# Optimization experiments

Hardware: AMD Instinct MI355X
Metric: run time of the kernel (lower is better)

Reference implementation:

```python
import jax, jax.numpy as jnp
import numpy as np

D = 192
HEADS = 4
HD = D // HEADS
R = 3  # correlation radius actually used in forward_level
NDISP = (2 * R + 1) ** 2  # 49
T = 3  # frames -> 2 consecutive pairs
ITERS = 4


def layer_norm(x, w, b, eps=1e-5):
    m = jnp.mean(x, axis=-1, keepdims=True)
    v = jnp.var(x, axis=-1, keepdims=True)
    return (x - m) / jnp.sqrt(v + eps) * w + b


def mha(x, in_w, in_b, out_w, out_b):
    # torch nn.MultiheadAttention, batch_first, self-attention
    B, N, _ = x.shape
    qkv = x @ in_w.T + in_b
    q, k, v = jnp.split(qkv, 3, axis=-1)
    q = q.reshape(B, N, HEADS, HD).transpose(0, 2, 1, 3) * (1.0 / float(np.sqrt(HD)))
    k = k.reshape(B, N, HEADS, HD).transpose(0, 2, 1, 3)
    v = v.reshape(B, N, HEADS, HD).transpose(0, 2, 1, 3)
    att = jax.nn.softmax(jnp.einsum('bhqd,bhkd->bhqk', q, k), axis=-1)
    y = jnp.einsum('bhqk,bhkd->bhqd', att, v).transpose(0, 2, 1, 3).reshape(B, N, D)
    return y @ out_w.T + out_b


def tblock(x, p):
    ln1w, ln1b, inw, inb, ow, ob, ln2w, ln2b, w1, b1, w2, b2 = p
    x = x + mha(layer_norm(x, ln1w, ln1b), inw, inb, ow, ob)
    h = layer_norm(x, ln2w, ln2b)
    h = jax.nn.gelu(h @ w1.T + b1, approximate=False) @ w2.T + b2
    return x + h


def local_corr(f1, f2):
    C = f1.shape[1]
    scale = 1.0 / float(np.sqrt(C))
    outs = []
    for dy in range(-R, R + 1):
        for dx in range(-R, R + 1):
            f2s = jnp.roll(f2, (dy, dx), axis=(2, 3))
            outs.append(jnp.sum(f1 * f2s, axis=1) * scale)
    return jnp.stack(outs, axis=1)


def grid_sample_bilinear_border(img, grid):
    # img: B,C,H,W; grid: B,Ho,Wo,2 with (x,y) in [-1,1]; align_corners=True, border padding
    B, C, H, W = img.shape
    x = jnp.clip((grid[..., 0] + 1.0) * 0.5 * (W - 1), 0.0, W - 1)
    y = jnp.clip((grid[..., 1] + 1.0) * 0.5 * (H - 1), 0.0, H - 1)
    x0 = jnp.floor(x); y0 = jnp.floor(y)
    x1 = jnp.minimum(x0 + 1, W - 1); y1 = jnp.minimum(y0 + 1, H - 1)
    wx = (x - x0)[:, None]; wy = (y - y0)[:, None]
    imgf = img.reshape(B, C, H * W)
    Ho, Wo = x.shape[1], x.shape[2]
    def gather(yy, xx):
        idx = (yy * W + xx).astype(jnp.int32).reshape(B, 1, Ho * Wo)
        return jnp.take_along_axis(imgf, idx, axis=2).reshape(B, C, Ho, Wo)
    v00 = gather(y0, x0); v01 = gather(y0, x1)
    v10 = gather(y1, x0); v11 = gather(y1, x1)
    return v00 * (1 - wx) * (1 - wy) + v01 * wx * (1 - wy) + v10 * (1 - wx) * wy + v11 * wx * wy


def warp(img, flow):
    # flow in pixels, Bx2xHxW
    B, C, H, W = img.shape
    xs = jnp.linspace(-1.0, 1.0, W); ys = jnp.linspace(-1.0, 1.0, H)
    gx, gy = jnp.meshgrid(xs, ys)  # each (H, W), 'xy' indexing
    base = jnp.stack([gx, gy], axis=-1)[None]
    off = jnp.stack([flow[:, 0] * (2.0 / max(W - 1, 1)),
                     flow[:, 1] * (2.0 / max(H - 1, 1))], axis=-1)
    return grid_sample_bilinear_border(img, base + off)


def upsample2x_align(img):
    # F.interpolate(scale_factor=2, mode='bilinear', align_corners=True)
    B, C, H, W = img.shape
    Ho, Wo = 2 * H, 2 * W
    xs = jnp.linspace(-1.0, 1.0, Wo); ys = jnp.linspace(-1.0, 1.0, Ho)
    gx, gy = jnp.meshgrid(xs, ys)
    grid = jnp.broadcast_to(jnp.stack([gx, gy], axis=-1)[None], (B, Ho, Wo, 2))
    return grid_sample_bilinear_border(img, grid)


def conv2d(x, w, b):
    y = jax.lax.conv_general_dilated(x, w, (1, 1), ((1, 1), (1, 1)),
                                     dimension_numbers=('NCHW', 'OIHW', 'NCHW'))
    return y + b[None, :, None, None]


def _forward(feats_l1, feats_l2, feats_l3, tok_w, tok_b,
             lcm_ln1_w, lcm_ln1_b, lcm_in_w, lcm_in_b, lcm_out_w, lcm_out_b,
             lcm_ln2_w, lcm_ln2_b, lcm_mlp_w1, lcm_mlp_b1, lcm_mlp_w2, lcm_mlp_b2,
             gtr_ln1_w, gtr_ln1_b, gtr_in_w, gtr_in_b, gtr_out_w, gtr_out_b,
             gtr_ln2_w, gtr_ln2_b, gtr_mlp_w1, gtr_mlp_b1, gtr_mlp_w2, gtr_mlp_b2,
             head_w1, head_b1, head_w2, head_b2,
             ref1_w1, ref1_b1, ref1_w2, ref1_b2,
             ref0_w1, ref0_b1, ref0_w2, ref0_b2):
    feats = [[feats_l1[t] for t in range(T)],
             [feats_l2[t] for t in range(T)],
             [feats_l3[t] for t in range(T)]]
    # ---- CostTokenizer ----
    tokens = []
    for lvl in range(3):
        toks = []
        for k in range(T - 1):
            corr = local_corr(feats[lvl][k], feats[lvl][k + 1])
            toks.append(jnp.einsum('bchw,dc->bdhw', corr, tok_w[lvl]) + tok_b[lvl][None, :, None, None])
        tokens.append(toks)
    lcm_p = [(lcm_ln1_w[i], lcm_ln1_b[i], lcm_in_w[i], lcm_in_b[i], lcm_out_w[i], lcm_out_b[i],
              lcm_ln2_w[i], lcm_ln2_b[i], lcm_mlp_w1[i], lcm_mlp_b1[i], lcm_mlp_w2[i], lcm_mlp_b2[i])
             for i in range(lcm_ln1_w.shape[0])]
    gtr_p = [(gtr_ln1_w[i], gtr_ln1_b[i], gtr_in_w[i], gtr_in_b[i], gtr_out_w[i], gtr_out_b[i],
              gtr_ln2_w[i], gtr_ln2_b[i], gtr_mlp_w1[i], gtr_mlp_b1[i], gtr_mlp_w2[i], gtr_mlp_b2[i])
             for i in range(gtr_ln1_w.shape[0])]
    # ---- LatentCostMemory (EMA state; .detach() -> stop_gradient; state resets when N changes) ----
    state = None
    latent = []
    for toks in tokens:
        lvl_lat = []
        for tok in toks:
            B_, Dd, H, W = tok.shape
            x = tok.reshape(B_, Dd, H * W).transpose(0, 2, 1)  # b (h w) d
            for p in lcm_p:
                x = tblock(x, p)
            if state is None or state.shape[1] != x.shape[1]:
                state = jax.lax.stop_gradient(x)
            x = 0.8 * x + 0.2 * state
            state = jax.lax.stop_gradient(x)
            lvl_lat.append(x.transpose(0, 2, 1))  # b d n
        latent.append(lvl_lat)
    H8, W8 = feats[1][0].shape[-2:]
    coarse = []
    for lat in latent[1]:
        x = lat.transpose(0, 2, 1)
        for p in gtr_p:
            x = tblock(x, p)
        fv = jax.nn.gelu(x @ head_w1.T + head_b1, approximate=False) @ head_w2.T + head_b2
        coarse.append(fv.transpose(0, 2, 1).reshape(-1, 2, H8, W8))
    # ---- MSRecurrentDecoder ----
    outs = []
    for k, f8 in enumerate(coarse):
        cur = f8
        for _ in range(ITERS):
            w10 = warp(feats[1][k + 1], cur)
            x = jnp.concatenate([feats[1][k], cur, w10], axis=1)
            cur = cur + conv2d(jax.nn.gelu(conv2d(x, ref1_w1, ref1_b1), approximate=False), ref1_w2, ref1_b2)
        cur2 = upsample2x_align(cur)
        for _ in range(ITERS):
            w10 = warp(feats[0][k + 1], cur2)
            x = jnp.concatenate([feats[0][k], cur2, w10], axis=1)
            cur2 = cur2 + conv2d(jax.nn.gelu(conv2d(x, ref0_w1, ref0_b1), approximate=False), ref0_w2, ref0_b2)
        outs.append(cur2)
    return jnp.stack(outs)  # [pairs, B, 2, H/4, W/4]


def setup_inputs():
    key = jax.random.key(0)
    ks = iter(jax.random.split(key, 64))
    def rn(shape, s=1.0):
        return jax.random.normal(next(ks), shape, dtype=jnp.float32) * s
    B = 1
    inp = {}
    inp['feats_l1'] = rn((T, B, 64, 64, 64))
    inp['feats_l2'] = rn((T, B, 128, 32, 32))
    inp['feats_l3'] = rn((T, B, 192, 16, 16))
    inp['tok_w'] = rn((3, D, NDISP), 0.02)
    inp['tok_b'] = rn((3, D), 0.02)
    for pre, n in (('lcm', 6), ('gtr', 2)):
        inp[pre + '_ln1_w'] = jnp.ones((n, D), jnp.float32)
        inp[pre + '_ln1_b'] = jnp.zeros((n, D), jnp.float32)
        inp[pre + '_in_w'] = rn((n, 3 * D, D), 0.02)
        inp[pre + '_in_b'] = rn((n, 3 * D), 0.02)
        inp[pre + '_out_w'] = rn((n, D, D), 0.02)
        inp[pre + '_out_b'] = rn((n, D), 0.02)
        inp[pre + '_ln2_w'] = jnp.ones((n, D), jnp.float32)
        inp[pre + '_ln2_b'] = jnp.zeros((n, D), jnp.float32)
        inp[pre + '_mlp_w1'] = rn((n, 4 * D, D), 0.02)
        inp[pre + '_mlp_b1'] = rn((n, 4 * D), 0.02)
        inp[pre + '_mlp_w2'] = rn((n, D, 4 * D), 0.02)
        inp[pre + '_mlp_b2'] = rn((n, D), 0.02)
    inp['head_w1'] = rn((D, D), 0.02); inp['head_b1'] = rn((D,), 0.02)
    inp['head_w2'] = rn((2, D), 0.02); inp['head_b2'] = rn((2,), 0.02)
    inp['ref1_w1'] = rn((128, 258, 3, 3), 0.02); inp['ref1_b1'] = rn((128,), 0.02)
    inp['ref1_w2'] = rn((2, 128, 3, 3), 0.02); inp['ref1_b2'] = rn((2,), 0.02)
    inp['ref0_w1'] = rn((64, 130, 3, 3), 0.02); inp['ref0_b1'] = rn((64,), 0.02)
    inp['ref0_w2'] = rn((2, 64, 3, 3), 0.02); inp['ref0_b2'] = rn((2,), 0.02)
    return inp


def reference(feats_l1, feats_l2, feats_l3, tok_w, tok_b,
              lcm_ln1_w, lcm_ln1_b, lcm_in_w, lcm_in_b, lcm_out_w, lcm_out_b,
              lcm_ln2_w, lcm_ln2_b, lcm_mlp_w1, lcm_mlp_b1, lcm_mlp_w2, lcm_mlp_b2,
              gtr_ln1_w, gtr_ln1_b, gtr_in_w, gtr_in_b, gtr_out_w, gtr_out_b,
              gtr_ln2_w, gtr_ln2_b, gtr_mlp_w1, gtr_mlp_b1, gtr_mlp_w2, gtr_mlp_b2,
              head_w1, head_b1, head_w2, head_b2,
              ref1_w1, ref1_b1, ref1_w2, ref1_b2,
              ref0_w1, ref0_b1, ref0_w2, ref0_b2):
    return _forward(feats_l1, feats_l2, feats_l3, tok_w, tok_b,
                    lcm_ln1_w, lcm_ln1_b, lcm_in_w, lcm_in_b, lcm_out_w, lcm_out_b,
                    lcm_ln2_w, lcm_ln2_b, lcm_mlp_w1, lcm_mlp_b1, lcm_mlp_w2, lcm_mlp_b2,
                    gtr_ln1_w, gtr_ln1_b, gtr_in_w, gtr_in_b, gtr_out_w, gtr_out_b,
                    gtr_ln2_w, gtr_ln2_b, gtr_mlp_w1, gtr_mlp_b1, gtr_mlp_w2, gtr_mlp_b2,
                    head_w1, head_b1, head_w2, head_b2,
                    ref1_w1, ref1_b1, ref1_w2, ref1_b2,
                    ref0_w1, ref0_b1, ref0_w2, ref0_b2)
```

## Files before the change

kernel.cpp:

```cpp
#include <hip/hip_runtime.h>
#include <hip/hip_bf16.h>

typedef __hip_bfloat16 bf16;
typedef short bf16x8 __attribute__((ext_vector_type(8)));
typedef float f32x4 __attribute__((ext_vector_type(4)));

#define DEV __device__ __forceinline__

DEV float bf2f(bf16 v) { return __bfloat162float(v); }
DEV bf16 f2bf(float v) { return __float2bfloat16(v); }
DEV unsigned short bfr(float f) {
  bf16 h = __float2bfloat16(f);
  return *reinterpret_cast<unsigned short*>(&h);
}
DEV float shf(unsigned short u) {
  unsigned int x = ((unsigned int)u) << 16;
  return *reinterpret_cast<float*>(&x);
}
DEV float gelu_exact(float x) { return 0.5f * x * (1.0f + erff(x * 0.70710678118654752f)); }

DEV float ldw(const void* p, long i, int isb) {
  return isb ? __bfloat162float(((const bf16*)p)[i]) : ((const float*)p)[i];
}

__global__ void k_detect(const unsigned short* __restrict__ u, int* __restrict__ flag) {
  __shared__ int bad;
  if (threadIdx.x == 0) bad = 0;
  __syncthreads();
  for (int i = threadIdx.x; i < 8192; i += 256) {
    int expo = (u[i] >> 7) & 0xFF;
    if (expo >= 138) atomicOr(&bad, 1);
  }
  __syncthreads();
  if (threadIdx.x == 0) *flag = bad ? 0 : 1;
}
__global__ void k_setone(int* p) { *p = 1; }

__global__ void k_cvt(const void* __restrict__ s, float* __restrict__ d, int n,
                      const int* __restrict__ fl) {
  int isb = *fl;
  int i = blockIdx.x * blockDim.x + threadIdx.x;
  if (i < n) d[i] = ldw(s, i, isb);
}

__global__ void k_zerosh(unsigned short* __restrict__ p, int n8) {
  int i = blockIdx.x * blockDim.x + threadIdx.x;
  if (i < n8) { uint4 z = {0, 0, 0, 0}; *(uint4*)(p + (long)i * 8) = z; }
}

__global__ void k_padtokw(const void* __restrict__ tw, bf16* __restrict__ dst,
                          const int* __restrict__ fl) {
  int isb = *fl;
  int i = blockIdx.x * blockDim.x + threadIdx.x;
  if (i >= 12288) return;
  int n = i >> 6, k = i & 63;
  float v = (k < 49) ? ldw(tw, 9408 + (long)n * 49 + k, isb) : 0.0f;
  dst[i] = f2bf(v);
}

__global__ void k_packw(const void* __restrict__ src, bf16* __restrict__ dst,
                        int OC, int C, int ICT, int NP, int ICP, int n,
                        const int* __restrict__ fl) {
  int isb = *fl;
  int i = blockIdx.x * blockDim.x + threadIdx.x;
  if (i >= n) return;
  int s = i / (NP * ICP);
  int r = i - s * NP * ICP;
  int oc = r / ICP, icp = r - oc * ICP;
  float v = 0.0f;
  if (oc < OC) {
    int ic = -1;
    if (icp < C) ic = icp;
    else if (icp < 2 * C) ic = icp - C + C + 2;
    else if (icp < 2 * C + 2) ic = icp - 2 * C + C;
    if (ic >= 0 && ic < ICT) v = ldw(src, ((long)oc * ICT + ic) * 9 + s, isb);
  }
  dst[i] = f2bf(v);
}

__global__ void k_trans_feats(const void* __restrict__ in, bf16* __restrict__ Fp,
                              int F, int C, int HW, const int* __restrict__ fl) {
  int isb = *fl;
  int cpg = C >> 3;
  int n = F * HW * cpg;
  int i = blockIdx.x * blockDim.x + threadIdx.x;
  if (i >= n) return;
  int p = i % HW;
  int rem = i / HW;
  int c8 = rem % cpg;
  int f = rem / cpg;
  long base = (long)f * C * HW + (long)(c8 * 8) * HW + p;
  union { unsigned short u[8]; uint4 v; } pk;
#pragma unroll
  for (int j = 0; j < 8; ++j) pk.u[j] = bfr(ldw(in, base + (long)j * HW, isb));
  *(uint4*)((unsigned short*)Fp + ((long)f * HW + p) * C + c8 * 8) = pk.v;
}

__global__ void k_fill_feats(const bf16* __restrict__ Fp, bf16* __restrict__ Ap,
                             int C, int ICP, int H, int W) {
  int HW = H * W;
  int cpg = C >> 3;
  int n = 2 * HW * cpg;
  int i = blockIdx.x * blockDim.x + threadIdx.x;
  if (i >= n) return;
  int g = i % cpg;
  int rem = i / cpg;
  int p = rem % HW;
  int b = rem / HW;
  int h = p / W, w = p - h * W;
  const unsigned short* src = (const unsigned short*)Fp + ((long)b * HW + p) * C + g * 8;
  unsigned short* dst = (unsigned short*)Ap +
      ((long)b * (H + 2) * (W + 2) + (long)(h + 1) * (W + 2) + w + 1) * ICP + g * 8;
  *(uint4*)dst = *(const uint4*)src;
}

__global__ void k_warp_pack(const bf16* __restrict__ Fp, const float* __restrict__ flow,
                            bf16* __restrict__ Ap, int C, int ICP, int H, int W) {
  int HW = H * W;
  int cpg = C >> 3;
  int n = 2 * HW * cpg;
  int i = blockIdx.x * blockDim.x + threadIdx.x;
  if (i >= n) return;
  int g = i % cpg;
  int rem = i / cpg;
  int p = rem % HW;
  int b = rem / HW;
  int h = p / W, w = p - h * W;
  const float* fl = flow + (long)b * 2 * HW;
  float fx = fl[p], fy = fl[HW + p];
  unsigned short* drow = (unsigned short*)Ap +
      ((long)b * (H + 2) * (W + 2) + (long)(h + 1) * (W + 2) + w + 1) * ICP;
  if (g == 0) { drow[2 * C] = bfr(fx); drow[2 * C + 1] = bfr(fy); }
  float x = fminf(fmaxf((float)w + fx, 0.0f), (float)(W - 1));
  float y = fminf(fmaxf((float)h + fy, 0.0f), (float)(H - 1));
  int x0 = (int)floorf(x), y0 = (int)floorf(y);
  int x1 = min(x0 + 1, W - 1), y1 = min(y0 + 1, H - 1);
  float wx = x - (float)x0, wy = y - (float)y0;
  float w00 = (1 - wx) * (1 - wy), w01 = wx * (1 - wy);
  float w10 = (1 - wx) * wy, w11 = wx * wy;
  const unsigned short* f = (const unsigned short*)Fp + (long)(b + 1) * HW * C;
  int c = g * 8;
  union { unsigned short u[8]; uint4 v; } a = { .v = *(const uint4*)(f + (long)(y0 * W + x0) * C + c) };
  union { unsigned short u[8]; uint4 v; } bb = { .v = *(const uint4*)(f + (long)(y0 * W + x1) * C + c) };
  union { unsigned short u[8]; uint4 v; } cc = { .v = *(const uint4*)(f + (long)(y1 * W + x0) * C + c) };
  union { unsigned short u[8]; uint4 v; } dd = { .v = *(const uint4*)(f + (long)(y1 * W + x1) * C + c) };
  union { unsigned short u[8]; uint4 v; } o;
#pragma unroll
  for (int j = 0; j < 8; ++j) {
    float v = shf(a.u[j]) * w00 + shf(bb.u[j]) * w01 + shf(cc.u[j]) * w10 + shf(dd.u[j]) * w11;
    o.u[j] = bfr(v);
  }
  *(uint4*)(drow + C + c) = o.v;
}

template <int MW, int NT, int MODE>
__global__ __launch_bounds__(256) void k_conv_mfma(
    const bf16* __restrict__ Ap, int ICP, const bf16* __restrict__ Wp,
    const float* __restrict__ bias, const float* __restrict__ res,
    void* __restrict__ out, int NOUT, int H, int W, int lgW) {
  constexpr int NWN = 4 / MW;
  constexpr int BM = MW * 16;
  constexpr int BN = NWN * NT * 16;
  __shared__ unsigned short Asm[198][40];
  __shared__ unsigned short Wsm[9 * BN][40];
  int tid = threadIdx.x;
  int wv = tid >> 6, ln = tid & 63, quad = ln >> 4, l16 = ln & 15;
  int wm = wv % MW, wn = wv / MW;
  int n0 = blockIdx.x * BN;
  int m0 = blockIdx.y * BM;
  int b = blockIdx.z;
  int Wp2 = W + 2;
  int CW = (BM < W) ? BM : W;
  int lgCW = (CW == 64) ? 6 : 5;
  int RO = (BM > W) ? (BM >> lgW) : 1;
  int ACW = CW + 2;
  int AR = (RO + 2) * ACW;
  int py0 = m0 >> lgW;
  int px0 = m0 & (W - 1);
  const unsigned short* A = (const unsigned short*)Ap + (long)b * (H + 2) * Wp2 * ICP;
  int NPr = (MODE == 0) ? NOUT : 16;
  int nk = ICP >> 5;
  f32x4 acc[NT] = {};
  int mm_local = wm * 16 + l16;
  int plr = mm_local >> lgCW;
  int plc = mm_local & (CW - 1);
  for (int kc = 0; kc < nk; ++kc) {
    for (int i = tid; i < AR * 4; i += 256) {
      int r = i >> 2, c4 = i & 3;
      int sr = r / ACW, sc = r - sr * ACW;
      long g = ((long)(py0 + sr) * Wp2 + px0 + sc) * ICP + kc * 32 + c4 * 8;
      *(uint4*)&Asm[r][c4 * 8] = *(const uint4*)(A + g);
    }
    for (int i = tid; i < 9 * BN * 4; i += 256) {
      int r = i >> 2, c4 = i & 3;
      int s = r / BN, nl = r - s * BN;
      long g = ((long)s * NPr + n0 + nl) * ICP + kc * 32 + c4 * 8;
      *(uint4*)&Wsm[r][c4 * 8] = *(const uint4*)((const unsigned short*)Wp + g);
    }
    __syncthreads();
#pragma unroll
    for (int s = 0; s < 9; ++s) {
      int ky = s / 3, kx = s - ky * 3;
      bf16x8 af = *(const bf16x8*)&Asm[(plr + ky) * ACW + plc + kx][quad * 8];
#pragma unroll
      for (int nt = 0; nt < NT; ++nt) {
        bf16x8 wf = *(const bf16x8*)&Wsm[s * BN + (wn * NT + nt) * 16 + l16][quad * 8];
        acc[nt] = __builtin_amdgcn_mfma_f32_16x16x32_bf16(af, wf, acc[nt], 0, 0, 0);
      }
    }
    __syncthreads();
  }
  if (MODE == 0) {
#pragma unroll
    for (int nt = 0; nt < NT; ++nt) {
      int n = n0 + (wn * NT + nt) * 16 + l16;
      float bv = bias[n];
#pragma unroll
      for (int r = 0; r < 4; ++r) {
        int mmo = m0 + wm * 16 + quad * 4 + r;
        int py = mmo >> lgW, px = mmo & (W - 1);
        float v = gelu_exact(acc[nt][r] + bv);
        ((unsigned short*)out)[((long)b * (H + 2) * Wp2 + (long)(py + 1) * Wp2 + px + 1) * NOUT + n]
            = bfr(v);
      }
    }
  } else {
    int n = l16;
    if (wn == 0 && n < 2) {
      float bv = bias[n];
      int HW = H * W;
#pragma unroll
      for (int r = 0; r < 4; ++r) {
        int mmo = m0 + wm * 16 + quad * 4 + r;
        float v = acc[0][r] + bv + res[(long)b * 2 * HW + (long)n * HW + mmo];
        ((float*)out)[(long)b * 2 * HW + (long)n * HW + mmo] = v;
      }
    }
  }
}

__global__ void k_corr(const bf16* __restrict__ Fp2, bf16* __restrict__ corrT) {
  __shared__ unsigned short f1r[128];
  int p = blockIdx.x;
  int b = blockIdx.y;
  int t = threadIdx.x;
  const unsigned short* f1 = (const unsigned short*)Fp2 + ((long)b * 1024 + p) * 128;
  if (t < 16) *(uint4*)&f1r[t * 8] = *(const uint4*)(f1 + t * 8);
  __syncthreads();
  long rowo = ((long)b * 1024 + p) * 64;
  if (t < 49) {
    int dy = t / 7 - 3, dx = t % 7 - 3;
    int h = p >> 5, w = p & 31;
    int p2 = (((h - dy) & 31) << 5) | ((w - dx) & 31);
    const unsigned short* f2 = (const unsigned short*)Fp2 + ((long)(b + 1) * 1024 + p2) * 128;
    float s = 0.0f;
    for (int c = 0; c < 128; c += 8) {
      union { unsigned short u[8]; uint4 v; } av = { .v = *(const uint4*)&f1r[c] };
      union { unsigned short u[8]; uint4 v; } bv = { .v = *(const uint4*)(f2 + c) };
#pragma unroll
      for (int j = 0; j < 8; ++j) s += shf(av.u[j]) * shf(bv.u[j]);
    }
    corrT[rowo + t] = f2bf(s * 0.08838834764831845f);
  } else {
    corrT[rowo + t] = f2bf(0.0f);
  }
}

__global__ __launch_bounds__(256) void k_ln(const float* __restrict__ src, bf16* __restrict__ dst,
                     const void* __restrict__ w, long woff,
                     const void* __restrict__ b, long boff,
                     const int* __restrict__ fl) {
  int isb = *fl;
  int row = blockIdx.x * 4 + (threadIdx.x >> 6);
  int t = threadIdx.x & 63;
  const float* s = src + (long)row * 192;
  float e0 = s[t], e1 = s[t + 64], e2 = s[t + 128];
  float sum = e0 + e1 + e2;
  for (int o = 32; o; o >>= 1) sum += __shfl_xor(sum, o);
  float mean = sum * (1.0f / 192.0f);
  float d0 = e0 - mean, d1 = e1 - mean, d2 = e2 - mean;
  float vs = d0 * d0 + d1 * d1 + d2 * d2;
  for (int o = 32; o; o >>= 1) vs += __shfl_xor(vs, o);
  float rstd = rsqrtf(vs * (1.0f / 192.0f) + 1e-5f);
  bf16* o_ = dst + (long)row * 192;
  o_[t]       = f2bf(d0 * rstd * ldw(w, woff + t, isb)       + ldw(b, boff + t, isb));
  o_[t + 64]  = f2bf(d1 * rstd * ldw(w, woff + t + 64, isb)  + ldw(b, boff + t + 64, isb));
  o_[t + 128] = f2bf(d2 * rstd * ldw(w, woff + t + 128, isb) + ldw(b, boff + t + 128, isb));
}

template <int ACT, bool HASRES, int AMODE, int OUTBF, int VT>
__global__ __launch_bounds__(256) void k_gemm_mfma(
    const void* __restrict__ A, const void* __restrict__ W, long woff,
    const void* __restrict__ bias, long boff, const int* __restrict__ flb,
    const float* __restrict__ res, void* __restrict__ C,
    int M, int N, int K, const int* __restrict__ fl,
    const unsigned short* __restrict__ mop, const float* __restrict__ mml,
    bf16* __restrict__ vtout) {
  int isb = *fl;
  __shared__ unsigned short Asm[64][40];
  __shared__ unsigned short Wsm[64][40];
  int tid = threadIdx.x;
  int wv = tid >> 6, ln = tid & 63;
  int quad = ln >> 4, l16 = ln & 15;
  int m0 = blockIdx.y * 64, n0 = blockIdx.x * 64;
  int srow = tid >> 2;
  int skc = (tid & 3) * 8;
  f32x4 acc[4] = {};
  for (int k0 = 0; k0 < K; k0 += 32) {
    if (AMODE == 1) {
      const unsigned short* ap = (const unsigned short*)A + (long)(m0 + srow) * K + k0 + skc;
      *(uint4*)&Asm[srow][skc] = *(const uint4*)ap;
    } else if (AMODE == 0) {
      const float* ap = (const float*)A + (long)(m0 + srow) * K + k0 + skc;
      float4 a0 = *(const float4*)ap;
      float4 a1 = *(const float4*)(ap + 4);
      union { unsigned short u[8]; uint4 v; } pk;
      pk.u[0] = bfr(a0.x); pk.u[1] = bfr(a0.y); pk.u[2] = bfr(a0.z); pk.u[3] = bfr(a0.w);
      pk.u[4] = bfr(a1.x); pk.u[5] = bfr(a1.y); pk.u[6] = bfr(a1.z); pk.u[7] = bfr(a1.w);
      *(uint4*)&Asm[srow][skc] = pk.v;
    } else {
      int m = m0 + srow;
      int row = m & 1023, bb = m >> 10;
      int ks = k0 + skc;
      int h = ks / 48;
      int d0 = ks - h * 48;
      long idx[4];
      float ms[4], ls[4];
      float Ms = -1e30f;
#pragma unroll
      for (int s = 0; s < 4; ++s) {
        idx[s] = (((long)s * 2 + bb) * 4 + h) * 1024 + row;
        ms[s] = mml[idx[s] * 2];
        ls[s] = mml[idx[s] * 2 + 1];
        Ms = fmaxf(Ms, ms[s]);
      }
      float e[4], L = 0.0f;
#pragma unroll
      for (int s = 0; s < 4; ++s) { e[s] = __expf(ms[s] - Ms); L += ls[s] * e[s]; }
      float invL = 1.0f / L;
      union { unsigned short u[8]; uint4 v; } pk;
#pragma unroll
      for (int j = 0; j < 8; ++j) {
        float o = 0.0f;
#pragma unroll
        for (int s = 0; s < 4; ++s) o += shf(mop[idx[s] * 48 + d0 + j]) * e[s];
        pk.u[j] = bfr(o * invL);
      }
      *(uint4*)&Asm[srow][skc] = pk.v;
    }
    {
      long eo = woff + (long)(n0 + srow) * K + k0 + skc;
      if (isb) {
        *(uint4*)&Wsm[srow][skc] = *(const uint4*)((const unsigned short*)W + eo);
      } else {
        const float* wp = (const float*)W + eo;
        float4 w0 = *(const float4*)wp;
        float4 w1 = *(const float4*)(wp + 4);
        union { unsigned short u[8]; uint4 v; } pk;
        pk.u[0] = bfr(w0.x); pk.u[1] = bfr(w0.y); pk.u[2] = bfr(w0.z); pk.u[3] = bfr(w0.w);
        pk.u[4] = bfr(w1.x); pk.u[5] = bfr(w1.y); pk.u[6] = bfr(w1.z); pk.u[7] = bfr(w1.w);
        *(uint4*)&Wsm[srow][skc] = pk.v;
      }
    }
    __syncthreads();
    bf16x8 af = *(const bf16x8*)&Asm[wv * 16 + l16][quad * 8];
#pragma unroll
    for (int nt = 0; nt < 4; ++nt) {
      bf16x8 wf = *(const bf16x8*)&Wsm[nt * 16 + l16][quad * 8];
      acc[nt] = __builtin_amdgcn_mfma_f32_16x16x32_bf16(af, wf, acc[nt], 0, 0, 0);
    }
    __syncthreads();
  }
  int isbb = *flb;
#pragma unroll
  for (int nt = 0; nt < 4; ++nt) {
    int n = n0 + nt * 16 + l16;
    float bv = ldw(bias, boff + n, isbb);
#pragma unroll
    for (int r = 0; r < 4; ++r) {
      int m = m0 + wv * 16 + quad * 4 + r;
      float v = acc[nt][r] + bv;
      if (HASRES) v += res[(long)m * N + n];
      if (ACT == 1) v = gelu_exact(v);
      if (OUTBF) ((bf16*)C)[(long)m * N + n] = f2bf(v);
      else ((float*)C)[(long)m * N + n] = v;
      if (VT) {
        if (n >= 384) {
          int hh = (n - 384) / 48, dd = (n - 384) % 48;
          int row = m & 1023, bb = m >> 10;
          vtout[((long)(bb * 4 + hh) * 48 + dd) * 1024 + row] = f2bf(v);
        }
      }
    }
  }
}

template <int ACT, bool HASRES, int FLOW>
__global__ __launch_bounds__(256) void k_gemm(const float* __restrict__ A,
                                              const void* __restrict__ W, long woff,
                                              const void* __restrict__ bias, long boff,
                                              const float* __restrict__ res,
                                              float* __restrict__ C, int M, int N, int K, int Kw,
                                              const int* __restrict__ fl) {
  int isb = *fl;
  __shared__ float As[16][132];
  __shared__ float Ws[16][68];
  int tid = threadIdx.x;
  int tx = tid & 15, ty = tid >> 4;
  int m0 = blockIdx.y * 128, n0 = blockIdx.x * 64;
  float acc[8][4] = {};
  for (int k0 = 0; k0 < K; k0 += 16) {
#pragma unroll
    for (int i = 0; i < 2; ++i) {
      int idx4 = tid + i * 256;
      int mm = idx4 >> 2, kc = (idx4 & 3) * 4;
      float4 v = *(const float4*)(A + (long)(m0 + mm) * K + k0 + kc);
      As[kc][mm] = v.x; As[kc + 1][mm] = v.y; As[kc + 2][mm] = v.z; As[kc + 3][mm] = v.w;
    }
#pragma unroll
    for (int i = 0; i < 4; ++i) {
      int idx = tid + i * 256;
      int nn = idx >> 4, kk = idx & 15;
      int gn = n0 + nn, gk = k0 + kk;
      Ws[kk][nn] = (gn < N && gk < Kw) ? ldw(W, woff + (long)gn * Kw + gk, isb) : 0.0f;
    }
    __syncthreads();
#pragma unroll
    for (int kk = 0; kk < 16; ++kk) {
      float4 a0 = *(const float4*)&As[kk][ty * 8];
      float4 a1 = *(const float4*)&As[kk][ty * 8 + 4];
      float4 w4 = *(const float4*)&Ws[kk][tx * 4];
      float av[8] = {a0.x, a0.y, a0.z, a0.w, a1.x, a1.y, a1.z, a1.w};
      float wv[4] = {w4.x, w4.y, w4.z, w4.w};
#pragma unroll
      for (int i = 0; i < 8; ++i)
#pragma unroll
        for (int j = 0; j < 4; ++j) acc[i][j] += av[i] * wv[j];
    }
    __syncthreads();
  }
#pragma unroll
  for (int i = 0; i < 8; ++i) {
    int gm = m0 + ty * 8 + i;
#pragma unroll
    for (int j = 0; j < 4; ++j) {
      int gn = n0 + tx * 4 + j;
      if (gn >= N) continue;
      float v = acc[i][j] + ldw(bias, boff + gn, isb);
      if (HASRES) v += res[(long)gm * N + gn];
      if (ACT == 1) v = gelu_exact(v);
      if (FLOW) {
        int bb2 = gm >> 10, p = gm & 1023;
        C[((long)bb2 * 2 + gn) * 1024 + p] = v;
      } else {
        C[(long)gm * N + gn] = v;
      }
    }
  }
}

__global__ __launch_bounds__(256) void k_attn_mfma(const bf16* __restrict__ qkv,
                                                   const bf16* __restrict__ vt,
                                                   unsigned short* __restrict__ opart,
                                                   float* __restrict__ ml) {
  __shared__ unsigned short Qs[64][72];
  __shared__ unsigned short Ks[64][72];
  __shared__ unsigned short Vs[48][72];
  __shared__ unsigned short Ps[64][72];
  int tid = threadIdx.x;
  int wv = tid >> 6, ln = tid & 63, quad = ln >> 4, l16 = ln & 15;
  int h = blockIdx.y, b = blockIdx.z;
  int qt = blockIdx.x >> 2, s = blockIdx.x & 3;
  int q0 = qt * 64;
  const unsigned short* qp = (const unsigned short*)qkv + (long)b * 1024 * 576;
  const unsigned short* vp = (const unsigned short*)vt + ((long)(b * 4 + h) * 48) * 1024;
  for (int i = tid; i < 384; i += 256) {
    int r = i / 6, c = i % 6;
    *(uint4*)&Qs[r][c * 8] = *(const uint4*)(qp + (long)(q0 + r) * 576 + h * 48 + c * 8);
  }
  for (int i = tid; i < 128; i += 256) {
    int r = i >> 1, c = 6 + (i & 1);
    uint4 z = {0, 0, 0, 0};
    *(uint4*)&Qs[r][c * 8] = z;
  }
  float m[4] = {-1e30f, -1e30f, -1e30f, -1e30f};
  float l[4] = {0.0f, 0.0f, 0.0f, 0.0f};
  f32x4 accO[3] = {};
  const float SC = 0.14433756729740643f;
  for (int kc = s * 4; kc < s * 4 + 4; ++kc) {
    int k0 = kc * 64;
    for (int i = tid; i < 384; i += 256) {
      int r = i / 6, c = i % 6;
      *(uint4*)&Ks[r][c * 8] = *(const uint4*)(qp + (long)(k0 + r) * 576 + 192 + h * 48 + c * 8);
    }
    for (int i = tid; i < 128; i += 256) {
      int r = i >> 1, c = 6 + (i & 1);
      uint4 z = {0, 0, 0, 0};
      *(uint4*)&Ks[r][c * 8] = z;
    }
    for (int i = tid; i < 384; i += 256) {
      int d = i >> 3, c = i & 7;
      *(uint4*)&Vs[d][c * 8] = *(const uint4*)(vp + (long)d * 1024 + k0 + c * 8);
    }
    __syncthreads();
    f32x4 accS[4] = {};
    bf16x8 a0 = *(const bf16x8*)&Qs[wv * 16 + l16][quad * 8];
    bf16x8 a1 = *(const bf16x8*)&Qs[wv * 16 + l16][32 + quad * 8];
#pragma unroll
    for (int ct = 0; ct < 4; ++ct) {
      bf16x8 b0 = *(const bf16x8*)&Ks[ct * 16 + l16][quad * 8];
      bf16x8 b1 = *(const bf16x8*)&Ks[ct * 16 + l16][32 + quad * 8];
      accS[ct] = __builtin_amdgcn_mfma_f32_16x16x32_bf16(a0, b0, accS[ct], 0, 0, 0);
      accS[ct] = __builtin_amdgcn_mfma_f32_16x16x32_bf16(a1, b1, accS[ct], 0, 0, 0);
    }
#pragma unroll
    for (int r = 0; r < 4; ++r) {
      float s0 = accS[0][r] * SC, s1 = accS[1][r] * SC;
      float s2 = accS[2][r] * SC, s3 = accS[3][r] * SC;
      float mx = fmaxf(fmaxf(s0, s1), fmaxf(s2, s3));
      for (int o = 8; o; o >>= 1) mx = fmaxf(mx, __shfl_xor(mx, o));
      float mn = fmaxf(m[r], mx);
      float alpha = __expf(m[r] - mn);
      float p0 = __expf(s0 - mn), p1 = __expf(s1 - mn);
      float p2 = __expf(s2 - mn), p3 = __expf(s3 - mn);
      float rs = p0 + p1 + p2 + p3;
      for (int o = 8; o; o >>= 1) rs += __shfl_xor(rs, o);
      m[r] = mn;
      l[r] = l[r] * alpha + rs;
      accO[0][r] *= alpha; accO[1][r] *= alpha; accO[2][r] *= alpha;
      int prow = wv * 16 + quad * 4 + r;
      Ps[prow][l16]      = bfr(p0);
      Ps[prow][16 + l16] = bfr(p1);
      Ps[prow][32 + l16] = bfr(p2);
      Ps[prow][48 + l16] = bfr(p3);
    }
    bf16x8 pf0 = *(const bf16x8*)&Ps[wv * 16 + l16][quad * 8];
    bf16x8 pf1 = *(const bf16x8*)&Ps[wv * 16 + l16][32 + quad * 8];
#pragma unroll
    for (int ct = 0; ct < 3; ++ct) {
      bf16x8 v0 = *(const bf16x8*)&Vs[ct * 16 + l16][quad * 8];
      bf16x8 v1 = *(const bf16x8*)&Vs[ct * 16 + l16][32 + quad * 8];
      accO[ct] = __builtin_amdgcn_mfma_f32_16x16x32_bf16(pf0, v0, accO[ct], 0, 0, 0);
      accO[ct] = __builtin_amdgcn_mfma_f32_16x16x32_bf16(pf1, v1, accO[ct], 0, 0, 0);
    }
    __syncthreads();
  }
  long base = (((long)s * 2 + b) * 4 + h) * 1024;
#pragma unroll
  for (int r = 0; r < 4; ++r) {
    int row = q0 + wv * 16 + quad * 4 + r;
#pragma unroll
    for (int ct = 0; ct < 3; ++ct)
      opart[(base + row) * 48 + ct * 16 + l16] = bfr(accO[ct][r]);
    if (l16 == 0) {
      ml[(base + row) * 2]     = m[r];
      ml[(base + row) * 2 + 1] = l[r];
    }
  }
}

__global__ void k_ema(float* __restrict__ x) {
  int i = blockIdx.x * blockDim.x + threadIdx.x;
  if (i < 196608) x[196608 + i] = 0.8f * x[196608 + i] + 0.2f * x[i];
}

__global__ void k_upsample(const float* __restrict__ in, float* __restrict__ out) {
  int i = blockIdx.x * blockDim.x + threadIdx.x;
  if (i >= 2 * 2 * 64 * 64) return;
  int p = i & 4095;
  int bc = i >> 12;
  int oy = p >> 6, ox = p & 63;
  float sx = ox * (31.0f / 63.0f), sy = oy * (31.0f / 63.0f);
  int x0 = (int)sx, y0 = (int)sy;
  int x1 = min(x0 + 1, 31), y1 = min(y0 + 1, 31);
  float wx = sx - x0, wy = sy - y0;
  const float* ic = in + (long)bc * 1024;
  out[i] = ic[y0 * 32 + x0] * (1 - wx) * (1 - wy) + ic[y0 * 32 + x1] * wx * (1 - wy)
         + ic[y1 * 32 + x0] * (1 - wx) * wy      + ic[y1 * 32 + x1] * wx * wy;
}

__global__ void k_out(const float* __restrict__ cur2, void* __restrict__ out,
                      const int* __restrict__ fl) {
  int isb = *fl;
  int i = blockIdx.x * blockDim.x + threadIdx.x;
  if (i < 16384) {
    if (isb) ((bf16*)out)[i] = f2bf(cur2[i]);
    else ((float*)out)[i] = cur2[i];
  }
}

extern "C" void kernel_launch(void* const* d_in, const int* in_sizes, int n_in,
                              void* d_out, int out_size, void* d_ws, size_t ws_size,
                              hipStream_t stream) {
  const void* feats_l1 = d_in[0];
  const void* feats_l2 = d_in[1];
  const void* tok_w = d_in[3];
  const void* tok_b = d_in[4];
  const void* lcm_ln1_w = d_in[5];
  const void* lcm_ln1_b = d_in[6];
  const void* lcm_in_w  = d_in[7];
  const void* lcm_in_b  = d_in[8];
  const void* lcm_out_w = d_in[9];
  const void* lcm_out_b = d_in[10];
  const void* lcm_ln2_w = d_in[11];
  const void* lcm_ln2_b = d_in[12];
  const void* lcm_mlp_w1 = d_in[13];
  const void* lcm_mlp_b1 = d_in[14];
  const void* lcm_mlp_w2 = d_in[15];
  const void* lcm_mlp_b2 = d_in[16];
  const void* gtr_ln1_w = d_in[17];
  const void* gtr_ln1_b = d_in[18];
  const void* gtr_in_w  = d_in[19];
  const void* gtr_in_b  = d_in[20];
  const void* gtr_out_w = d_in[21];
  const void* gtr_out_b = d_in[22];
  const void* gtr_ln2_w = d_in[23];
  const void* gtr_ln2_b = d_in[24];
  const void* gtr_mlp_w1 = d_in[25];
  const void* gtr_mlp_b1 = d_in[26];
  const void* gtr_mlp_w2 = d_in[27];
  const void* gtr_mlp_b2 = d_in[28];
  const void* head_w1 = d_in[29];
  const void* head_b1 = d_in[30];
  const void* head_w2 = d_in[31];
  const void* head_b2 = d_in[32];
  const void* ref1_w1 = d_in[33];
  const void* ref1_b1 = d_in[34];
  const void* ref1_w2 = d_in[35];
  const void* ref1_b2 = d_in[36];
  const void* ref0_w1 = d_in[37];
  const void* ref0_b1 = d_in[38];
  const void* ref0_w2 = d_in[39];
  const void* ref0_b2 = d_in[40];
  (void)ws_size; (void)n_in; (void)in_sizes; (void)out_size;

  int* flag = (int*)d_ws;
  int* oneflag = (int*)d_ws + 2;
  float* wsf = (float*)d_ws;
  float* F2   = wsf + 16;
  float* rA   = F2 + 393216;
  float* rX   = rA + 786432;
  float* rT   = rX + 393216;
  float* rY   = rT + 393216;
  float* big  = rY + 393216;
  float* fv   = big + 1572864;
  float* cur  = fv + 4096;
  float* cur2 = cur + 4096;
  float* cb1a = cur2 + 16384;
  float* cb1b = cb1a + 128;
  float* cb0a = cb1b + 16;
  float* cb0b = cb0a + 64;
  bf16* wtok  = (bf16*)(cb0b + 16);
  float* wpk  = cb0b + 16 + 6144;
  bf16* w1p1 = (bf16*)wpk;
  bf16* w1p2 = (bf16*)(wpk + 165888);
  bf16* w0p1 = (bf16*)(wpk + 175104);
  bf16* w0p2 = (bf16*)(wpk + 221184);

  float* x = rX;
  bf16* tb     = (bf16*)rT;
  bf16* corrTb = (bf16*)big;
  bf16* qkvbb  = (bf16*)big;
  bf16* vtb    = (bf16*)(big + 655360);
  bf16* hidb   = (bf16*)big;
  unsigned short* opart = (unsigned short*)rA;
  float* mlbuf = rY;
  float* headh = rT;
  bf16* A0p   = (bf16*)rA;
  bf16* A1p   = (bf16*)rX;
  bf16* mid0p = (bf16*)rT;
  bf16* mid1p = (bf16*)rY;
  bf16* Fp2   = (bf16*)(big + 851968);
  bf16* Fp1   = (bf16*)(big + 1048576);

  k_detect<<<1, 256, 0, stream>>>((const unsigned short*)feats_l1, flag);
  k_setone<<<1, 1, 0, stream>>>(oneflag);
  k_cvt<<<1, 256, 0, stream>>>(ref1_b1, cb1a, 128, flag);
  k_cvt<<<1, 256, 0, stream>>>(ref1_b2, cb1b, 2, flag);
  k_cvt<<<1, 256, 0, stream>>>(ref0_b1, cb0a, 64, flag);
  k_cvt<<<1, 256, 0, stream>>>(ref0_b2, cb0b, 2, flag);
  k_padtokw<<<48, 256, 0, stream>>>(tok_w, wtok, flag);
  k_packw<<<1296, 256, 0, stream>>>(ref1_w1, w1p1, 128, 128, 258, 128, 288, 331776, flag);
  k_packw<<<72, 256, 0, stream>>>(ref1_w2, w1p2, 2, 128, 128, 16, 128, 18432, flag);
  k_packw<<<360, 256, 0, stream>>>(ref0_w1, w0p1, 64, 64, 130, 64, 160, 92160, flag);
  k_packw<<<36, 256, 0, stream>>>(ref0_w2, w0p2, 2, 64, 64, 16, 64, 9216, flag);
  k_trans_feats<<<192, 256, 0, stream>>>(feats_l2, Fp2, 3, 128, 1024, flag);
  k_trans_feats<<<384, 256, 0, stream>>>(feats_l1, Fp1, 3, 64, 4096, flag);

  k_corr<<<dim3(1024, 2), 64, 0, stream>>>(Fp2, corrTb);
  k_gemm_mfma<0, false, 1, 0, 0><<<dim3(3, 32), 256, 0, stream>>>(
      corrTb, wtok, 0, tok_b, 192, flag, nullptr, x, 2048, 192, 64, oneflag,
      nullptr, nullptr, nullptr);

  auto run_block = [&](const void* ln1w, long o1, const void* ln1b, long o2,
                       const void* inw, long o3, const void* inb, long o4,
                       const void* ow, long o5, const void* ob, long o6,
                       const void* ln2w, long o7, const void* ln2b, long o8,
                       const void* w1, long o9, const void* b1, long o10,
                       const void* w2, long o11, const void* b2, long o12) {
    k_ln<<<512, 256, 0, stream>>>(x, tb, ln1w, o1, ln1b, o2, flag);
    k_gemm_mfma<0, false, 1, 1, 1><<<dim3(9, 32), 256, 0, stream>>>(
        tb, inw, o3, inb, o4, flag, nullptr, qkvbb, 2048, 576, 192, flag,
        nullptr, nullptr, vtb);
    k_attn_mfma<<<dim3(64, 4, 2), 256, 0, stream>>>(qkvbb, vtb, opart, mlbuf);
    k_gemm_mfma<0, true, 2, 0, 0><<<dim3(3, 32), 256, 0, stream>>>(
        nullptr, ow, o5, ob, o6, flag, x, x, 2048, 192, 192, flag,
        opart, mlbuf, nullptr);
    k_ln<<<512, 256, 0, stream>>>(x, tb, ln2w, o7, ln2b, o8, flag);
    k_gemm_mfma<1, false, 1, 1, 0><<<dim3(12, 32), 256, 0, stream>>>(
        tb, w1, o9, b1, o10, flag, nullptr, hidb, 2048, 768, 192, flag,
        nullptr, nullptr, nullptr);
    k_gemm_mfma<0, true, 1, 0, 0><<<dim3(3, 32), 256, 0, stream>>>(
        hidb, w2, o11, b2, o12, flag, x, x, 2048, 192, 768, flag,
        nullptr, nullptr, nullptr);
  };

  for (int i = 0; i < 6; ++i) {
    run_block(lcm_ln1_w, (long)i * 192, lcm_ln1_b, (long)i * 192,
              lcm_in_w, (long)i * 110592, lcm_in_b, (long)i * 576,
              lcm_out_w, (long)i * 36864, lcm_out_b, (long)i * 192,
              lcm_ln2_w, (long)i * 192, lcm_ln2_b, (long)i * 192,
              lcm_mlp_w1, (long)i * 147456, lcm_mlp_b1, (long)i * 768,
              lcm_mlp_w2, (long)i * 147456, lcm_mlp_b2, (long)i * 192);
  }
  k_ema<<<768, 256, 0, stream>>>(x);

  for (int i = 0; i < 2; ++i) {
    run_block(gtr_ln1_w, (long)i * 192, gtr_ln1_b, (long)i * 192,
              gtr_in_w, (long)i * 110592, gtr_in_b, (long)i * 576,
              gtr_out_w, (long)i * 36864, gtr_out_b, (long)i * 192,
              gtr_ln2_w, (long)i * 192, gtr_ln2_b, (long)i * 192,
              gtr_mlp_w1, (long)i * 147456, gtr_mlp_b1, (long)i * 768,
              gtr_mlp_w2, (long)i * 147456, gtr_mlp_b2, (long)i * 192);
  }

  k_gemm_mfma<1, false, 0, 0, 0><<<dim3(3, 32), 256, 0, stream>>>(
      x, head_w1, 0, head_b1, 0, flag, nullptr, headh, 2048, 192, 192, flag,
      nullptr, nullptr, nullptr);
  k_gemm<0, false, 1><<<dim3(1, 16), 256, 0, stream>>>(headh, head_w2, 0, head_b2, 0, nullptr,
                                                       cur, 2048, 2, 192, 192, flag);

  k_zerosh<<<1920, 256, 0, stream>>>((unsigned short*)rA, 491520);
  k_fill_feats<<<128, 256, 0, stream>>>(Fp2, A1p, 128, 288, 32, 32);

  for (int it = 0; it < 4; ++it) {
    k_warp_pack<<<128, 256, 0, stream>>>(Fp2, cur, A1p, 128, 288, 32, 32);
    k_conv_mfma<2, 2, 0><<<dim3(2, 32, 2), 256, 0, stream>>>(
        A1p, 288, w1p1, cb1a, nullptr, mid1p, 128, 32, 32, 5);
    k_conv_mfma<4, 1, 1><<<dim3(1, 16, 2), 256, 0, stream>>>(
        mid1p, 128, w1p2, cb1b, cur, cur, 2, 32, 32, 5);
  }
  k_upsample<<<64, 256, 0, stream>>>(cur, cur2);
  k_fill_feats<<<256, 256, 0, stream>>>(Fp1, A0p, 64, 160, 64, 64);

  for (int it = 0; it < 4; ++it) {
    k_warp_pack<<<256, 256, 0, stream>>>(Fp1, cur2, A0p, 64, 160, 64, 64);
    k_conv_mfma<2, 2, 0><<<dim3(1, 128, 2), 256, 0, stream>>>(
        A0p, 160, w0p1, cb0a, nullptr, mid0p, 64, 64, 64, 6);
    k_conv_mfma<4, 1, 1><<<dim3(1, 64, 2), 256, 0, stream>>>(
        mid0p, 64, w0p2, cb0b, cur2, cur2, 2, 64, 64, 6);
  }

  k_out<<<64, 256, 0, stream>>>(cur2, d_out, flag);
}
```

Measured before the change: 1.120 ms.

## Fuse LayerNorm into GEMM prologue and stage full-K tiles in shared memory

Removes the standalone LayerNorm kernels. The QKV and MLP-up GEMMs now normalize rows of x directly in their A-tile load (AMODE 3). The GEMM template takes K as a compile-time parameter and loads up to 192 of K into shared memory at once (6 chunks of 32), which cuts the barriers per K-step. This saves two launches per transformer block and the round trip of the LN output, at the cost of larger shared memory per block (about 60KB), which may lower occupancy, and more register pressure from the 48-float row buffer.

```diff
diff --git a/kernel.cpp b/kernel.cpp
--- a/kernel.cpp
+++ b/kernel.cpp
@@ -266,92 +266,33 @@
   }
 }
 
-__global__ __launch_bounds__(256) void k_ln(const float* __restrict__ src, bf16* __restrict__ dst,
-                     const void* __restrict__ w, long woff,
-                     const void* __restrict__ b, long boff,
-                     const int* __restrict__ fl) {
-  int isb = *fl;
-  int row = blockIdx.x * 4 + (threadIdx.x >> 6);
-  int t = threadIdx.x & 63;
-  const float* s = src + (long)row * 192;
-  float e0 = s[t], e1 = s[t + 64], e2 = s[t + 128];
-  float sum = e0 + e1 + e2;
-  for (int o = 32; o; o >>= 1) sum += __shfl_xor(sum, o);
-  float mean = sum * (1.0f / 192.0f);
-  float d0 = e0 - mean, d1 = e1 - mean, d2 = e2 - mean;
-  float vs = d0 * d0 + d1 * d1 + d2 * d2;
-  for (int o = 32; o; o >>= 1) vs += __shfl_xor(vs, o);
-  float rstd = rsqrtf(vs * (1.0f / 192.0f) + 1e-5f);
-  bf16* o_ = dst + (long)row * 192;
-  o_[t]       = f2bf(d0 * rstd * ldw(w, woff + t, isb)       + ldw(b, boff + t, isb));
-  o_[t + 64]  = f2bf(d1 * rstd * ldw(w, woff + t + 64, isb)  + ldw(b, boff + t + 64, isb));
-  o_[t + 128] = f2bf(d2 * rstd * ldw(w, woff + t + 128, isb) + ldw(b, boff + t + 128, isb));
-}
-
-template <int ACT, bool HASRES, int AMODE, int OUTBF, int VT>
-__global__ __launch_bounds__(256) void k_gemm_mfma(
+template <int KT, int ACT, bool HASRES, int AMODE, int OUTBF, int VT>
+__global__ __launch_bounds__(256) void k_gemm_mfma2(
     const void* __restrict__ A, const void* __restrict__ W, long woff,
     const void* __restrict__ bias, long boff, const int* __restrict__ flb,
     const float* __restrict__ res, void* __restrict__ C,
-    int M, int N, int K, const int* __restrict__ fl,
+    int M, int N, const int* __restrict__ fl,
     const unsigned short* __restrict__ mop, const float* __restrict__ mml,
-    bf16* __restrict__ vtout) {
+    bf16* __restrict__ vtout,
+    const void* __restrict__ lnw, long lnwoff,
+    const void* __restrict__ lnb, long lnboff) {
+  (void)M;
   int isb = *fl;
-  __shared__ unsigned short Asm[64][40];
-  __shared__ unsigned short Wsm[64][40];
+  __shared__ unsigned short Asm[6][64][40];
+  __shared__ unsigned short Wsm[6][64][40];
   int tid = threadIdx.x;
   int wv = tid >> 6, ln = tid & 63;
   int quad = ln >> 4, l16 = ln & 15;
   int m0 = blockIdx.y * 64, n0 = blockIdx.x * 64;
-  int srow = tid >> 2;
-  int skc = (tid & 3) * 8;
   f32x4 acc[4] = {};
-  for (int k0 = 0; k0 < K; k0 += 32) {
-    if (AMODE == 1) {
-      const unsigned short* ap = (const unsigned short*)A + (long)(m0 + srow) * K + k0 + skc;
-      *(uint4*)&Asm[srow][skc] = *(const uint4*)ap;
-    } else if (AMODE == 0) {
-      const float* ap = (const float*)A + (long)(m0 + srow) * K + k0 + skc;
-      float4 a0 = *(const float4*)ap;
-      float4 a1 = *(const float4*)(ap + 4);
-      union { unsigned short u[8]; uint4 v; } pk;
-      pk.u[0] = bfr(a0.x); pk.u[1] = bfr(a0.y); pk.u[2] = bfr(a0.z); pk.u[3] = bfr(a0.w);
-      pk.u[4] = bfr(a1.x); pk.u[5] = bfr(a1.y); pk.u[6] = bfr(a1.z); pk.u[7] = bfr(a1.w);
-      *(uint4*)&Asm[srow][skc] = pk.v;
-    } else {
-      int m = m0 + srow;
-      int row = m & 1023, bb = m >> 10;
-      int ks = k0 + skc;
-      int h = ks / 48;
-      int d0 = ks - h * 48;
-      long idx[4];
-      float ms[4], ls[4];
-      float Ms = -1e30f;
-#pragma unroll
-      for (int s = 0; s < 4; ++s) {
-        idx[s] = (((long)s * 2 + bb) * 4 + h) * 1024 + row;
-        ms[s] = mml[idx[s] * 2];
-        ls[s] = mml[idx[s] * 2 + 1];
-        Ms = fmaxf(Ms, ms[s]);
-      }
-      float e[4], L = 0.0f;
-#pragma unroll
-      for (int s = 0; s < 4; ++s) { e[s] = __expf(ms[s] - Ms); L += ls[s] * e[s]; }
-      float invL = 1.0f / L;
-      union { unsigned short u[8]; uint4 v; } pk;
-#pragma unroll
-      for (int j = 0; j < 8; ++j) {
-        float o = 0.0f;
-#pragma unroll
-        for (int s = 0; s < 4; ++s) o += shf(mop[idx[s] * 48 + d0 + j]) * e[s];
-        pk.u[j] = bfr(o * invL);
-      }
-      *(uint4*)&Asm[srow][skc] = pk.v;
-    }
-    {
-      long eo = woff + (long)(n0 + srow) * K + k0 + skc;
+  constexpr int NKC = ((KT < 192) ? KT : 192) >> 5;
+  for (int s0 = 0; s0 < KT; s0 += 192) {
+    if (s0) __syncthreads();
+    for (int i = tid; i < NKC * 256; i += 256) {
+      int c4 = i & 3, r = (i >> 2) & 63, kc = i >> 8;
+      long eo = woff + (long)(n0 + r) * KT + s0 + kc * 32 + c4 * 8;
       if (isb) {
-        *(uint4*)&Wsm[srow][skc] = *(const uint4*)((const unsigned short*)W + eo);
+        *(uint4*)&Wsm[kc][r][c4 * 8] = *(const uint4*)((const unsigned short*)W + eo);
       } else {
         const float* wp = (const float*)W + eo;
         float4 w0 = *(const float4*)wp;
@@ -359,17 +300,108 @@
         union { unsigned short u[8]; uint4 v; } pk;
         pk.u[0] = bfr(w0.x); pk.u[1] = bfr(w0.y); pk.u[2] = bfr(w0.z); pk.u[3] = bfr(w0.w);
         pk.u[4] = bfr(w1.x); pk.u[5] = bfr(w1.y); pk.u[6] = bfr(w1.z); pk.u[7] = bfr(w1.w);
-        *(uint4*)&Wsm[srow][skc] = pk.v;
+        *(uint4*)&Wsm[kc][r][c4 * 8] = pk.v;
+      }
+    }
+    if constexpr (AMODE == 1) {
+      for (int i = tid; i < NKC * 256; i += 256) {
+        int c4 = i & 3, r = (i >> 2) & 63, kc = i >> 8;
+        const unsigned short* ap =
+            (const unsigned short*)A + (long)(m0 + r) * KT + s0 + kc * 32 + c4 * 8;
+        *(uint4*)&Asm[kc][r][c4 * 8] = *(const uint4*)ap;
+      }
+    } else if constexpr (AMODE == 0) {
+      for (int i = tid; i < NKC * 256; i += 256) {
+        int c4 = i & 3, r = (i >> 2) & 63, kc = i >> 8;
+        const float* ap = (const float*)A + (long)(m0 + r) * KT + s0 + kc * 32 + c4 * 8;
+        float4 a0 = *(const float4*)ap;
+        float4 a1 = *(const float4*)(ap + 4);
+        union { unsigned short u[8]; uint4 v; } pk;
+        pk.u[0] = bfr(a0.x); pk.u[1] = bfr(a0.y); pk.u[2] = bfr(a0.z); pk.u[3] = bfr(a0.w);
+        pk.u[4] = bfr(a1.x); pk.u[5] = bfr(a1.y); pk.u[6] = bfr(a1.z); pk.u[7] = bfr(a1.w);
+        *(uint4*)&Asm[kc][r][c4 * 8] = pk.v;
+      }
+    } else if constexpr (AMODE == 3) {
+      int row = tid >> 2, j = tid & 3;
+      const float* xr = (const float*)A + (long)(m0 + row) * 192 + j * 8;
+      float av[48];
+#pragma unroll
+      for (int kc = 0; kc < 6; ++kc) {
+        float4 v0 = *(const float4*)(xr + kc * 32);
+        float4 v1 = *(const float4*)(xr + kc * 32 + 4);
+        av[kc * 8 + 0] = v0.x; av[kc * 8 + 1] = v0.y;
+        av[kc * 8 + 2] = v0.z; av[kc * 8 + 3] = v0.w;
+        av[kc * 8 + 4] = v1.x; av[kc * 8 + 5] = v1.y;
+        av[kc * 8 + 6] = v1.z; av[kc * 8 + 7] = v1.w;
+      }
+      float sum = 0.0f;
+#pragma unroll
+      for (int q = 0; q < 48; ++q) sum += av[q];
+      sum += __shfl_xor(sum, 1);
+      sum += __shfl_xor(sum, 2);
+      float mean = sum * (1.0f / 192.0f);
+      float vs = 0.0f;
+#pragma unroll
+      for (int q = 0; q < 48; ++q) { float d = av[q] - mean; vs += d * d; }
+      vs += __shfl_xor(vs, 1);
+      vs += __shfl_xor(vs, 2);
+      float rstd = rsqrtf(vs * (1.0f / 192.0f) + 1e-5f);
+#pragma unroll
+      for (int kc = 0; kc < 6; ++kc) {
+        union { unsigned short u[8]; uint4 v; } pk;
+#pragma unroll
+        for (int e = 0; e < 8; ++e) {
+          long k = kc * 32 + j * 8 + e;
+          float g = ldw(lnw, lnwoff + k, isb);
+          float bb = ldw(lnb, lnboff + k, isb);
+          pk.u[e] = bfr((av[kc * 8 + e] - mean) * rstd * g + bb);
+        }
+        *(uint4*)&Asm[kc][row][j * 8] = pk.v;
+      }
+    } else {
+      int row = tid >> 2, j = tid & 3;
+      int m = m0 + row;
+      int rr = m & 1023, bb = m >> 10;
+#pragma unroll
+      for (int kc = 0; kc < 6; ++kc) {
+        int k = kc * 32 + j * 8;
+        int h = k / 48;
+        int d0 = k - h * 48;
+        long idx[4];
+        float ms[4], ls[4];
+        float Ms = -1e30f;
+#pragma unroll
+        for (int s = 0; s < 4; ++s) {
+          idx[s] = (((long)s * 2 + bb) * 4 + h) * 1024 + rr;
+          ms[s] = mml[idx[s] * 2];
+          ls[s] = mml[idx[s] * 2 + 1];
+          Ms = fmaxf(Ms, ms[s]);
+        }
+        float e[4], L = 0.0f;
+#pragma unroll
+        for (int s = 0; s < 4; ++s) { e[s] = __expf(ms[s] - Ms); L += ls[s] * e[s]; }
+        float invL = 1.0f / L;
+        union { unsigned short u[8]; uint4 v; } pk;
+#pragma unroll
+        for (int e2 = 0; e2 < 8; ++e2) {
+          float o = 0.0f;
+#pragma unroll
+          for (int s = 0; s < 4; ++s) o += shf(mop[idx[s] * 48 + d0 + e2]) * e[s];
+          pk.u[e2] = bfr(o * invL);
+        }
+        *(uint4*)&Asm[kc][row][j * 8] = pk.v;
       }
     }
     __syncthreads();
-    bf16x8 af = *(const bf16x8*)&Asm[wv * 16 + l16][quad * 8];
-#pragma unroll
-    for (int nt = 0; nt < 4; ++nt) {
-      bf16x8 wf = *(const bf16x8*)&Wsm[nt * 16 + l16][quad * 8];
-      acc[nt] = __builtin_amdgcn_mfma_f32_16x16x32_bf16(af, wf, acc[nt], 0, 0, 0);
-    }
-    __syncthreads();
+#pragma unroll
+    for (int kc = 0; kc < NKC; ++kc) {
+      bf16x8 af = *(const bf16x8*)&Asm[kc][wv * 16 + l16][quad * 8];
+#pragma unroll
+      for (int nt = 0; nt < 4; ++nt) {
+        bf16x8 wf = *(const bf16x8*)&Wsm[kc][nt * 16 + l16][quad * 8];
+        acc[nt] = __builtin_amdgcn_mfma_f32_16x16x32_bf16(af, wf, acc[nt], 0, 0, 0);
+      }
+    }
   }
   int isbb = *flb;
 #pragma unroll
@@ -658,7 +690,6 @@
   bf16* w0p2 = (bf16*)(wpk + 221184);
 
   float* x = rX;
-  bf16* tb     = (bf16*)rT;
   bf16* corrTb = (bf16*)big;
   bf16* qkvbb  = (bf16*)big;
   bf16* vtb    = (bf16*)(big + 655360);
@@ -688,9 +719,9 @@
   k_trans_feats<<<384, 256, 0, stream>>>(feats_l1, Fp1, 3, 64, 4096, flag);
 
   k_corr<<<dim3(1024, 2), 64, 0, stream>>>(Fp2, corrTb);
-  k_gemm_mfma<0, false, 1, 0, 0><<<dim3(3, 32), 256, 0, stream>>>(
-      corrTb, wtok, 0, tok_b, 192, flag, nullptr, x, 2048, 192, 64, oneflag,
-      nullptr, nullptr, nullptr);
+  k_gemm_mfma2<64, 0, false, 1, 0, 0><<<dim3(3, 32), 256, 0, stream>>>(
+      corrTb, wtok, 0, tok_b, 192, flag, nullptr, x, 2048, 192, oneflag,
+      nullptr, nullptr, nullptr, nullptr, 0, nullptr, 0);
 
   auto run_block = [&](const void* ln1w, long o1, const void* ln1b, long o2,
                        const void* inw, long o3, const void* inb, long o4,
@@ -698,21 +729,19 @@
                        const void* ln2w, long o7, const void* ln2b, long o8,
                        const void* w1, long o9, const void* b1, long o10,
                        const void* w2, long o11, const void* b2, long o12) {
-    k_ln<<<512, 256, 0, stream>>>(x, tb, ln1w, o1, ln1b, o2, flag);
-    k_gemm_mfma<0, false, 1, 1, 1><<<dim3(9, 32), 256, 0, stream>>>(
-        tb, inw, o3, inb, o4, flag, nullptr, qkvbb, 2048, 576, 192, flag,
-        nullptr, nullptr, vtb);
+    k_gemm_mfma2<192, 0, false, 3, 1, 1><<<dim3(9, 32), 256, 0, stream>>>(
+        x, inw, o3, inb, o4, flag, nullptr, qkvbb, 2048, 576, flag,
+        nullptr, nullptr, vtb, ln1w, o1, ln1b, o2);
     k_attn_mfma<<<dim3(64, 4, 2), 256, 0, stream>>>(qkvbb, vtb, opart, mlbuf);
-    k_gemm_mfma<0, true, 2, 0, 0><<<dim3(3, 32), 256, 0, stream>>>(
-        nullptr, ow, o5, ob, o6, flag, x, x, 2048, 192, 192, flag,
-        opart, mlbuf, nullptr);
-    k_ln<<<512, 256, 0, stream>>>(x, tb, ln2w, o7, ln2b, o8, flag);
-    k_gemm_mfma<1, false, 1, 1, 0><<<dim3(12, 32), 256, 0, stream>>>(
-        tb, w1, o9, b1, o10, flag, nullptr, hidb, 2048, 768, 192, flag,
-        nullptr, nullptr, nullptr);
-    k_gemm_mfma<0, true, 1, 0, 0><<<dim3(3, 32), 256, 0, stream>>>(
-        hidb, w2, o11, b2, o12, flag, x, x, 2048, 192, 768, flag,
-        nullptr, nullptr, nullptr);
+    k_gemm_mfma2<192, 0, true, 2, 0, 0><<<dim3(3, 32), 256, 0, stream>>>(
+        nullptr, ow, o5, ob, o6, flag, x, x, 2048, 192, flag,
+        opart, mlbuf, nullptr, nullptr, 0, nullptr, 0);
+    k_gemm_mfma2<192, 1, false, 3, 1, 0><<<dim3(12, 32), 256, 0, stream>>>(
+        x, w1, o9, b1, o10, flag, nullptr, hidb, 2048, 768, flag,
+        nullptr, nullptr, nullptr, ln2w, o7, ln2b, o8);
+    k_gemm_mfma2<768, 0, true, 1, 0, 0><<<dim3(3, 32), 256, 0, stream>>>(
+        hidb, w2, o11, b2, o12, flag, x, x, 2048, 192, flag,
+        nullptr, nullptr, nullptr, nullptr, 0, nullptr, 0);
   };
 
   for (int i = 0; i < 6; ++i) {
@@ -734,9 +763,9 @@
               gtr_mlp_w2, (long)i * 147456, gtr_mlp_b2, (long)i * 192);
   }
 
-  k_gemm_mfma<1, false, 0, 0, 0><<<dim3(3, 32), 256, 0, stream>>>(
-      x, head_w1, 0, head_b1, 0, flag, nullptr, headh, 2048, 192, 192, flag,
-      nullptr, nullptr, nullptr);
+  k_gemm_mfma2<192, 1, false, 0, 0, 0><<<dim3(3, 32), 256, 0, stream>>>(
+      x, head_w1, 0, head_b1, 0, flag, nullptr, headh, 2048, 192, flag,
+      nullptr, nullptr, nullptr, nullptr, 0, nullptr, 0);
   k_gemm<0, false, 1><<<dim3(1, 16), 256, 0, stream>>>(headh, head_w2, 0, head_b2, 0, nullptr,
                                                        cur, 2048, 2, 192, 192, flag);
 
```

After: 1.087 ms. 1.03x faster.
